# Kernel tuning notes

Hardware: AMD Instinct MI355X
Metric: run time of the kernel (lower is better)

Reference implementation:

```python
import jax, jax.numpy as jnp
import numpy as np


def setup_inputs() -> dict:
    key = jax.random.key(0)
    k1, k2 = jax.random.split(key)
    D, N, M = 256, 1024, 1024
    z_x = jax.random.normal(k1, (1, D, N), dtype=jnp.float32)
    z_y = jax.random.normal(k2, (1, D, M), dtype=jnp.float32)
    return {"z_x": z_x, "z_y": z_y}


def reference(z_x, z_y):
    # squeeze().t(): (1, d, N) -> (N, d)
    x = jnp.squeeze(z_x).T  # (N, d)
    y = jnp.squeeze(z_y).T  # (M, d)
    # L1 compare: s[i, j] = -sum_d |x[i, d] - y[j, d]|  -> (N, M)
    s = -jnp.sum(jnp.abs(x[:, None, :] - y[None, :, :]), axis=-1)
    a = jax.nn.softmax(s, axis=1)  # row-wise softmax
    b = jax.nn.softmax(s, axis=0)  # column-wise softmax
    a = a + b - a * b              # soft union of alignments
    return jnp.sum(a * s) / jnp.sum(a)
```

## Files before the change

### kernel.cpp

```cpp
#include <hip/hip_runtime.h>
#include <math.h>


#define DD 256
#define NN 1024
#define DS 4
#define CH (DD / DS)

__device__ __forceinline__ float waveMax(float v) {
  #pragma unroll
  for (int off = 32; off; off >>= 1) v = fmaxf(v, __shfl_xor(v, off, 64));
  return v;
}
__device__ __forceinline__ float waveSum(float v) {
  #pragma unroll
  for (int off = 32; off; off >>= 1) v += __shfl_xor(v, off, 64);
  return v;
}
__device__ __forceinline__ float blockMax(float v, float* red) {
  v = waveMax(v);
  __syncthreads();
  if ((threadIdx.x & 63) == 0) red[threadIdx.x >> 6] = v;
  __syncthreads();
  return fmaxf(fmaxf(red[0], red[1]), fmaxf(red[2], red[3]));
}
__device__ __forceinline__ float blockSum(float v, float* red) {
  v = waveSum(v);
  __syncthreads();
  if ((threadIdx.x & 63) == 0) red[threadIdx.x >> 6] = v;
  __syncthreads();
  return red[0] + red[1] + red[2] + red[3];
}


__global__ __launch_bounds__(256)
void scompute_kernel(const float* __restrict__ zx, const float* __restrict__ zy,
                     float* __restrict__ Sp, float* __restrict__ accum) {
  const int h  = blockIdx.z;
  const int i0 = blockIdx.y * 64;
  const int j0 = blockIdx.x * 128;
  const int t  = threadIdx.x;
  const int g  = t >> 5;
  const int c  = t & 31;
  if ((blockIdx.x | blockIdx.y | blockIdx.z) == 0 && t == 0) {
    accum[0] = 0.f; accum[1] = 0.f;
  }

  __shared__ float xs[CH * 64];
  {
    const float4* __restrict__ X4 = (const float4*)zx;
    float4* xs4 = (float4*)xs;
    #pragma unroll
    for (int k = t; k < CH * 16; k += 256)
      xs4[k] = X4[(h * CH + (k >> 4)) * (NN / 4) + (i0 >> 2) + (k & 15)];
  }
  __syncthreads();

  float acc[8][4];
  #pragma unroll
  for (int r = 0; r < 8; ++r)
    #pragma unroll
    for (int q = 0; q < 4; ++q) acc[r][q] = 0.f;

  const float4* __restrict__ yp =
      (const float4*)zy + (size_t)(h * CH) * (NN / 4) + (j0 >> 2) + c;
  #pragma unroll 4
  for (int d = 0; d < CH; ++d) {
    const float4 yv = yp[d * (NN / 4)];
    const float* xr = xs + d * 64 + g * 8;
    #pragma unroll
    for (int r = 0; r < 8; ++r) {
      const float xv = xr[r];
      acc[r][0] += fabsf(xv - yv.x);
      acc[r][1] += fabsf(xv - yv.y);
      acc[r][2] += fabsf(xv - yv.z);
      acc[r][3] += fabsf(xv - yv.w);
    }
  }

  float4* __restrict__ S4 = (float4*)Sp + (size_t)h * (NN * NN / 4);
  #pragma unroll
  for (int r = 0; r < 8; ++r)
    S4[(i0 + g * 8 + r) * (NN / 4) + (j0 >> 2) + c] =
        make_float4(acc[r][0], acc[r][1], acc[r][2], acc[r][3]);
}

__global__ __launch_bounds__(256)
void rowstats_kernel(float* __restrict__ Sp,
                     float* __restrict__ rmax, float* __restrict__ rsum) {
  __shared__ float red[4];
  const int t = threadIdx.x;
  const int row0 = blockIdx.x * 4;
  float4* S4 = (float4*)Sp;
  #pragma unroll
  for (int rr = 0; rr < 4; ++rr) {
    const int row = row0 + rr;
    float4 p = S4[row * (NN / 4) + t];
    #pragma unroll
    for (int hh = 1; hh < DS; ++hh) {
      const float4 q = S4[hh * (NN * NN / 4) + row * (NN / 4) + t];
      p.x += q.x; p.y += q.y; p.z += q.z; p.w += q.w;
    }
    S4[row * (NN / 4) + t] = p;
    float m = fmaxf(fmaxf(-p.x, -p.y), fmaxf(-p.z, -p.w));
    m = blockMax(m, red);
    float l = __expf(-p.x - m) + __expf(-p.y - m) +
              __expf(-p.z - m) + __expf(-p.w - m);
    l = blockSum(l, red);
    if (t == 0) { rmax[row] = m; rsum[row] = l; }
  }
}

__global__ __launch_bounds__(256)
void colstats_kernel(const float* __restrict__ Sp,
                     float* __restrict__ pm, float* __restrict__ ps) {
  const int t = threadIdx.x;
  const int r0 = blockIdx.x * 16;
  const float4* S4 = (const float4*)Sp;
  float4 m = make_float4(-1e30f, -1e30f, -1e30f, -1e30f);
  #pragma unroll 4
  for (int i = 0; i < 16; ++i) {
    const float4 p = S4[(r0 + i) * (NN / 4) + t];
    m.x = fmaxf(m.x, -p.x); m.y = fmaxf(m.y, -p.y);
    m.z = fmaxf(m.z, -p.z); m.w = fmaxf(m.w, -p.w);
  }
  float4 l = make_float4(0.f, 0.f, 0.f, 0.f);
  #pragma unroll 4
  for (int i = 0; i < 16; ++i) {
    const float4 p = S4[(r0 + i) * (NN / 4) + t];
    l.x += __expf(-p.x - m.x); l.y += __expf(-p.y - m.y);
    l.z += __expf(-p.z - m.z); l.w += __expf(-p.w - m.w);
  }
  ((float4*)pm)[blockIdx.x * (NN / 4) + t] = m;
  ((float4*)ps)[blockIdx.x * (NN / 4) + t] = l;
}

__global__ __launch_bounds__(256)
void colcombine_kernel(const float* __restrict__ pm, const float* __restrict__ ps,
                       float* __restrict__ cmax, float* __restrict__ csum) {
  const int j = blockIdx.x * 256 + threadIdx.x;
  float m = -1e30f;
  #pragma unroll 8
  for (int k = 0; k < 64; ++k) m = fmaxf(m, pm[k * NN + j]);
  float l = 0.f;
  #pragma unroll 8
  for (int k = 0; k < 64; ++k) l += __expf(pm[k * NN + j] - m) * ps[k * NN + j];
  cmax[j] = m; csum[j] = l;
}

__global__ __launch_bounds__(256)
void final_kernel(const float* __restrict__ Sp,
                  const float* __restrict__ rmax, const float* __restrict__ rsum,
                  const float* __restrict__ cmax, const float* __restrict__ csum,
                  float* __restrict__ accum) {
  __shared__ float redn[4], redd[4];
  const int t = threadIdx.x;
  const int row0 = blockIdx.x * 4;
  const float4* S4 = (const float4*)Sp;
  const float4 cm = ((const float4*)cmax)[t];
  const float4 cs = ((const float4*)csum)[t];
  float un = 0.f, ud = 0.f;
  #pragma unroll
  for (int rr = 0; rr < 4; ++rr) {
    const int row = row0 + rr;
    const float rm = rmax[row];
    const float ri = 1.f / rsum[row];
    const float4 p = S4[row * (NN / 4) + t];
    {
      const float s = -p.x;
      const float a = __expf(s - rm) * ri;
      const float b = __expf(s - cm.x) / cs.x;
      const float u = a + b - a * b;
      un += u * s; ud += u;
    }
    {
      const float s = -p.y;
      const float a = __expf(s - rm) * ri;
      const float b = __expf(s - cm.y) / cs.y;
      const float u = a + b - a * b;
      un += u * s; ud += u;
    }
    {
      const float s = -p.z;
      const float a = __expf(s - rm) * ri;
      const float b = __expf(s - cm.z) / cs.z;
      const float u = a + b - a * b;
      un += u * s; ud += u;
    }
    {
      const float s = -p.w;
      const float a = __expf(s - rm) * ri;
      const float b = __expf(s - cm.w) / cs.w;
      const float u = a + b - a * b;
      un += u * s; ud += u;
    }
  }
  un = waveSum(un); ud = waveSum(ud);
  if ((t & 63) == 0) { redn[t >> 6] = un; redd[t >> 6] = ud; }
  __syncthreads();
  if (t == 0) {
    atomicAdd(&accum[0], redn[0] + redn[1] + redn[2] + redn[3]);
    atomicAdd(&accum[1], redd[0] + redd[1] + redd[2] + redd[3]);
  }
}

__global__ void finalize_kernel(const float* __restrict__ accum, float* __restrict__ out) {
  out[0] = accum[0] / accum[1];
}


#define TJ  128
#define NCH (NN / TJ)
#define BLK 256

__global__ __launch_bounds__(BLK)
void stats2_kernel(const float* __restrict__ zx, const float* __restrict__ zy,
                   float* __restrict__ partM, float* __restrict__ partS) {
  const int side = blockIdx.z;
  const float* __restrict__ X = side ? zy : zx;
  const float* __restrict__ Y = side ? zx : zy;
  const int j0 = blockIdx.x * TJ;
  const int i0 = blockIdx.y * 8;
  const int t  = threadIdx.x;
  const int rg = t >> 5;
  const int c  = t & 31;

  __shared__ float xs[8 * DD];
  for (int k = t; k < 8 * DD; k += BLK)
    xs[k] = X[(k >> 3) * NN + i0 + (k & 7)];
  __syncthreads();

  const float4* __restrict__ Y4 = (const float4*)Y;
  const int yb = (j0 >> 2) + c;
  float4 acc = make_float4(0.f, 0.f, 0.f, 0.f);
  #pragma unroll 8
  for (int d = 0; d < DD; ++d) {
    const float4 yv = Y4[d * (NN / 4) + yb];
    const float xv = xs[d * 8 + rg];
    acc.x += fabsf(xv - yv.x);
    acc.y += fabsf(xv - yv.y);
    acc.z += fabsf(xv - yv.z);
    acc.w += fabsf(xv - yv.w);
  }

  float m = fmaxf(fmaxf(-acc.x, -acc.y), fmaxf(-acc.z, -acc.w));
  #pragma unroll
  for (int off = 16; off > 0; off >>= 1) m = fmaxf(m, __shfl_xor(m, off, 32));
  float p = __expf(-acc.x - m) + __expf(-acc.y - m) +
            __expf(-acc.z - m) + __expf(-acc.w - m);
  #pragma unroll
  for (int off = 16; off > 0; off >>= 1) p += __shfl_xor(p, off, 32);

  if (c == 0) {
    const int idx = side * (NCH * NN) + blockIdx.x * NN + (i0 + rg);
    partM[idx] = m;
    partS[idx] = p;
  }
}

__global__ __launch_bounds__(BLK)
void combine_kernel(const float* __restrict__ partM, const float* __restrict__ partS,
                    float* __restrict__ rmax, float* __restrict__ rsum,
                    float* __restrict__ cmax, float* __restrict__ csum,
                    float* __restrict__ accum) {
  const int gid = blockIdx.x * BLK + threadIdx.x;
  if (gid == 0) { accum[0] = 0.f; accum[1] = 0.f; }
  const int sd = gid >> 10;
  const int i  = gid & (NN - 1);
  float mk[NCH], sk[NCH];
  #pragma unroll
  for (int k = 0; k < NCH; ++k) {
    mk[k] = partM[sd * (NCH * NN) + k * NN + i];
    sk[k] = partS[sd * (NCH * NN) + k * NN + i];
  }
  float m = mk[0];
  #pragma unroll
  for (int k = 1; k < NCH; ++k) m = fmaxf(m, mk[k]);
  float s = 0.f;
  #pragma unroll
  for (int k = 0; k < NCH; ++k) s += __expf(mk[k] - m) * sk[k];
  if (sd == 0) { rmax[i] = m; rsum[i] = s; }
  else         { cmax[i] = m; csum[i] = s; }
}

__global__ __launch_bounds__(BLK)
void final2_kernel(const float* __restrict__ zx, const float* __restrict__ zy,
                   const float* __restrict__ rmax, const float* __restrict__ rsum,
                   const float* __restrict__ cmax, const float* __restrict__ csum,
                   float* __restrict__ accum) {
  const int j0 = blockIdx.x * TJ;
  const int i0 = blockIdx.y * 8;
  const int t  = threadIdx.x;
  const int rg = t >> 5;
  const int c  = t & 31;

  __shared__ float xs[8 * DD];
  __shared__ float redn[4], redd[4];
  for (int k = t; k < 8 * DD; k += BLK)
    xs[k] = zx[(k >> 3) * NN + i0 + (k & 7)];
  __syncthreads();

  const float4* __restrict__ Y4 = (const float4*)zy;
  const int yb = (j0 >> 2) + c;
  float4 acc = make_float4(0.f, 0.f, 0.f, 0.f);
  #pragma unroll 8
  for (int d = 0; d < DD; ++d) {
    const float4 yv = Y4[d * (NN / 4) + yb];
    const float xv = xs[d * 8 + rg];
    acc.x += fabsf(xv - yv.x);
    acc.y += fabsf(xv - yv.y);
    acc.z += fabsf(xv - yv.z);
    acc.w += fabsf(xv - yv.w);
  }

  const int i = i0 + rg;
  const float rm = rmax[i];
  const float ri = 1.f / rsum[i];
  const float4 cm = ((const float4*)cmax)[yb];
  const float4 cs = ((const float4*)csum)[yb];

  float un = 0.f, ud = 0.f;
  {
    const float s = -acc.x;
    const float a = __expf(s - rm) * ri;
    const float b = __expf(s - cm.x) / cs.x;
    const float u = a + b - a * b;
    un += u * s; ud += u;
  }
  {
    const float s = -acc.y;
    const float a = __expf(s - rm) * ri;
    const float b = __expf(s - cm.y) / cs.y;
    const float u = a + b - a * b;
    un += u * s; ud += u;
  }
  {
    const float s = -acc.z;
    const float a = __expf(s - rm) * ri;
    const float b = __expf(s - cm.z) / cs.z;
    const float u = a + b - a * b;
    un += u * s; ud += u;
  }
  {
    const float s = -acc.w;
    const float a = __expf(s - rm) * ri;
    const float b = __expf(s - cm.w) / cs.w;
    const float u = a + b - a * b;
    un += u * s; ud += u;
  }

  un = waveSum(un); ud = waveSum(ud);
  if ((t & 63) == 0) { redn[t >> 6] = un; redd[t >> 6] = ud; }
  __syncthreads();
  if (t == 0) {
    atomicAdd(&accum[0], redn[0] + redn[1] + redn[2] + redn[3]);
    atomicAdd(&accum[1], redd[0] + redd[1] + redd[2] + redd[3]);
  }
}


extern "C" void kernel_launch(void* const* d_in, const int* in_sizes, int n_in,
                              void* d_out, int out_size, void* d_ws, size_t ws_size,
                              hipStream_t stream) {
  const float* zx = (const float*)d_in[0];
  const float* zy = (const float*)d_in[1];
  float* ws  = (float*)d_ws;
  float* out = (float*)d_out;

  float* accum = ws;
  float* Sp    = ws + 16;
  float* pm    = Sp + DS * NN * NN;
  float* ps    = pm + 64 * NN;
  float* rmax  = ps + 64 * NN;
  float* rsum  = rmax + NN;
  float* cmax  = rsum + NN;
  float* csum  = cmax + NN;
  const size_t need = (size_t)((csum + NN) - ws) * sizeof(float);

  if (ws_size >= need) {
    dim3 g1(NN / 128, NN / 64, DS);
    scompute_kernel<<<g1, 256, 0, stream>>>(zx, zy, Sp, accum);
    rowstats_kernel<<<NN / 4, 256, 0, stream>>>(Sp, rmax, rsum);
    colstats_kernel<<<NN / 16, 256, 0, stream>>>(Sp, pm, ps);
    colcombine_kernel<<<NN / 256, 256, 0, stream>>>(pm, ps, cmax, csum);
    final_kernel<<<NN / 4, 256, 0, stream>>>(Sp, rmax, rsum, cmax, csum, accum);
    finalize_kernel<<<1, 1, 0, stream>>>(accum, out);
  } else {
    float* partM = ws + 16;
    float* partS = partM + 2 * NCH * NN;
    float* frmax = partS + 2 * NCH * NN;
    float* frsum = frmax + NN;
    float* fcmax = frsum + NN;
    float* fcsum = fcmax + NN;
    dim3 sgrid(NCH, NN / 8, 2);
    stats2_kernel<<<sgrid, BLK, 0, stream>>>(zx, zy, partM, partS);
    combine_kernel<<<(2 * NN) / BLK, BLK, 0, stream>>>(partM, partS,
                                                       frmax, frsum, fcmax, fcsum, accum);
    dim3 fgrid(NCH, NN / 8);
    final2_kernel<<<fgrid, BLK, 0, stream>>>(zx, zy, frmax, frsum, fcmax, fcsum, accum);
    finalize_kernel<<<1, 1, 0, stream>>>(accum, out);
  }
}
```

Baseline: 125.2 us.

## Fuse row/column softmax partial stats into distance kernel, drop split-D partials

The L1 distance kernel now computes the full D reduction per tile and a single S matrix, with Y tiles double-buffered in shared memory. It also emits per-tile row and column max/sum-exp partials, which removes the separate rowstats and colstats passes and the reads of four partial S copies. A single combine kernel merges the partials. The final kernel finishes the division through a last-block atomic counter, which drops the finalize launch. The grid shrinks to 256 blocks with launch_bounds(256,1), so occupancy and parallelism may be low relative to the earlier 512-block split-D launch.

Result: slower. 127.8 us (+2.1%).

```diff
diff --git a/kernel.cpp b/kernel.cpp
--- a/kernel.cpp
+++ b/kernel.cpp
@@ -4,8 +4,7 @@
 
 #define DD 256
 #define NN 1024
-#define DS 4
-#define CH (DD / DS)
+#define NQ 256
 
 __device__ __forceinline__ float waveMax(float v) {
   #pragma unroll
@@ -17,155 +16,168 @@
   for (int off = 32; off; off >>= 1) v += __shfl_xor(v, off, 64);
   return v;
 }
-__device__ __forceinline__ float blockMax(float v, float* red) {
-  v = waveMax(v);
-  __syncthreads();
-  if ((threadIdx.x & 63) == 0) red[threadIdx.x >> 6] = v;
-  __syncthreads();
-  return fmaxf(fmaxf(red[0], red[1]), fmaxf(red[2], red[3]));
-}
-__device__ __forceinline__ float blockSum(float v, float* red) {
-  v = waveSum(v);
-  __syncthreads();
-  if ((threadIdx.x & 63) == 0) red[threadIdx.x >> 6] = v;
-  __syncthreads();
-  return red[0] + red[1] + red[2] + red[3];
-}
-
+
+
+__global__ __launch_bounds__(256, 1)
+void scompute_kernel(const float* __restrict__ zx, const float* __restrict__ zy,
+                     float* __restrict__ S,
+                     float* __restrict__ pRM, float* __restrict__ pRL,
+                     float* __restrict__ pCM, float* __restrict__ pCL) {
+  const int bx = blockIdx.x;
+  const int by = blockIdx.y;
+  const int i0 = by * 16;
+  const int t  = threadIdx.x;
+  const int w  = t >> 6;
+  const int ln = t & 63;
+
+  __shared__ float xs[DD][16];
+  __shared__ float ys[2][8][256];
+  __shared__ float cmS[4][256];
+  __shared__ float clS[4][256];
+
+  const float4* __restrict__ X4 = (const float4*)zx;
+  const float4* __restrict__ Y4 = (const float4*)zy;
+
+  #pragma unroll
+  for (int i = 0; i < 4; ++i) {
+    const int k = t + i * 256;
+    const int d = k >> 2, rq = k & 3;
+    *(float4*)&xs[d][rq * 4] = X4[d * NQ + by * 4 + rq];
+  }
+
+  const int sd = t >> 6;
+  const int sq = t & 63;
+  {
+    const float4 q0 = Y4[(sd)     * NQ + bx * 64 + sq];
+    const float4 q1 = Y4[(4 + sd) * NQ + bx * 64 + sq];
+    *(float4*)&ys[0][sd][sq * 4]     = q0;
+    *(float4*)&ys[0][4 + sd][sq * 4] = q1;
+  }
+  __syncthreads();
+
+  float acc[4][4];
+  #pragma unroll
+  for (int r = 0; r < 4; ++r)
+    #pragma unroll
+    for (int c = 0; c < 4; ++c) acc[r][c] = 0.f;
+
+  #pragma unroll 1
+  for (int n = 0; n < DD / 8; ++n) {
+    const int buf = n & 1;
+    float4 p0, p1;
+    if (n < DD / 8 - 1) {
+      p0 = Y4[(8 * (n + 1) + sd)     * NQ + bx * 64 + sq];
+      p1 = Y4[(8 * (n + 1) + 4 + sd) * NQ + bx * 64 + sq];
+    }
+    #pragma unroll
+    for (int dd = 0; dd < 8; ++dd) {
+      const int d = n * 8 + dd;
+      const float4 xv = *(const float4*)&xs[d][w * 4];
+      const float4 yv = *(const float4*)&ys[buf][dd][ln * 4];
+      acc[0][0] += fabsf(xv.x - yv.x); acc[0][1] += fabsf(xv.x - yv.y);
+      acc[0][2] += fabsf(xv.x - yv.z); acc[0][3] += fabsf(xv.x - yv.w);
+      acc[1][0] += fabsf(xv.y - yv.x); acc[1][1] += fabsf(xv.y - yv.y);
+      acc[1][2] += fabsf(xv.y - yv.z); acc[1][3] += fabsf(xv.y - yv.w);
+      acc[2][0] += fabsf(xv.z - yv.x); acc[2][1] += fabsf(xv.z - yv.y);
+      acc[2][2] += fabsf(xv.z - yv.z); acc[2][3] += fabsf(xv.z - yv.w);
+      acc[3][0] += fabsf(xv.w - yv.x); acc[3][1] += fabsf(xv.w - yv.y);
+      acc[3][2] += fabsf(xv.w - yv.z); acc[3][3] += fabsf(xv.w - yv.w);
+    }
+    if (n < DD / 8 - 1) {
+      *(float4*)&ys[buf ^ 1][sd][sq * 4]     = p0;
+      *(float4*)&ys[buf ^ 1][4 + sd][sq * 4] = p1;
+    }
+    __syncthreads();
+  }
+
+  float4* __restrict__ S4 = (float4*)S;
+  #pragma unroll
+  for (int r = 0; r < 4; ++r)
+    S4[(i0 + w * 4 + r) * NQ + bx * 64 + ln] =
+        make_float4(acc[r][0], acc[r][1], acc[r][2], acc[r][3]);
+
+  #pragma unroll
+  for (int r = 0; r < 4; ++r) {
+    float m = fmaxf(fmaxf(-acc[r][0], -acc[r][1]), fmaxf(-acc[r][2], -acc[r][3]));
+    m = waveMax(m);
+    float l = __expf(-acc[r][0] - m) + __expf(-acc[r][1] - m) +
+              __expf(-acc[r][2] - m) + __expf(-acc[r][3] - m);
+    l = waveSum(l);
+    if (ln == 0) {
+      pRM[bx * NN + i0 + w * 4 + r] = m;
+      pRL[bx * NN + i0 + w * 4 + r] = l;
+    }
+  }
+
+  #pragma unroll
+  for (int c = 0; c < 4; ++c) {
+    float m = fmaxf(fmaxf(-acc[0][c], -acc[1][c]), fmaxf(-acc[2][c], -acc[3][c]));
+    float l = __expf(-acc[0][c] - m) + __expf(-acc[1][c] - m) +
+              __expf(-acc[2][c] - m) + __expf(-acc[3][c] - m);
+    cmS[w][ln * 4 + c] = m;
+    clS[w][ln * 4 + c] = l;
+  }
+  __syncthreads();
+  {
+    const int j = t;
+    const float m0 = cmS[0][j], m1 = cmS[1][j], m2 = cmS[2][j], m3 = cmS[3][j];
+    const float M = fmaxf(fmaxf(m0, m1), fmaxf(m2, m3));
+    const float L = clS[0][j] * __expf(m0 - M) + clS[1][j] * __expf(m1 - M) +
+                    clS[2][j] * __expf(m2 - M) + clS[3][j] * __expf(m3 - M);
+    pCM[by * NN + bx * 256 + j] = M;
+    pCL[by * NN + bx * 256 + j] = L;
+  }
+}
 
 __global__ __launch_bounds__(256)
-void scompute_kernel(const float* __restrict__ zx, const float* __restrict__ zy,
-                     float* __restrict__ Sp, float* __restrict__ accum) {
-  const int h  = blockIdx.z;
-  const int i0 = blockIdx.y * 64;
-  const int j0 = blockIdx.x * 128;
-  const int t  = threadIdx.x;
-  const int g  = t >> 5;
-  const int c  = t & 31;
-  if ((blockIdx.x | blockIdx.y | blockIdx.z) == 0 && t == 0) {
-    accum[0] = 0.f; accum[1] = 0.f;
-  }
-
-  __shared__ float xs[CH * 64];
-  {
-    const float4* __restrict__ X4 = (const float4*)zx;
-    float4* xs4 = (float4*)xs;
+void combine_kernel(const float* __restrict__ pRM, const float* __restrict__ pRL,
+                    const float* __restrict__ pCM, const float* __restrict__ pCL,
+                    float* __restrict__ rmax, float* __restrict__ rsum,
+                    float* __restrict__ cmax, float* __restrict__ csum,
+                    float* __restrict__ accum) {
+  const int b = blockIdx.x, t = threadIdx.x;
+  if (b == 0 && t == 0) {
+    accum[0] = 0.f; accum[1] = 0.f; ((unsigned int*)accum)[2] = 0u;
+  }
+  if (b < 4) {
+    const int r = b * 256 + t;
+    float mk[4], lk[4];
     #pragma unroll
-    for (int k = t; k < CH * 16; k += 256)
-      xs4[k] = X4[(h * CH + (k >> 4)) * (NN / 4) + (i0 >> 2) + (k & 15)];
-  }
-  __syncthreads();
-
-  float acc[8][4];
-  #pragma unroll
-  for (int r = 0; r < 8; ++r)
-    #pragma unroll
-    for (int q = 0; q < 4; ++q) acc[r][q] = 0.f;
-
-  const float4* __restrict__ yp =
-      (const float4*)zy + (size_t)(h * CH) * (NN / 4) + (j0 >> 2) + c;
-  #pragma unroll 4
-  for (int d = 0; d < CH; ++d) {
-    const float4 yv = yp[d * (NN / 4)];
-    const float* xr = xs + d * 64 + g * 8;
-    #pragma unroll
-    for (int r = 0; r < 8; ++r) {
-      const float xv = xr[r];
-      acc[r][0] += fabsf(xv - yv.x);
-      acc[r][1] += fabsf(xv - yv.y);
-      acc[r][2] += fabsf(xv - yv.z);
-      acc[r][3] += fabsf(xv - yv.w);
-    }
-  }
-
-  float4* __restrict__ S4 = (float4*)Sp + (size_t)h * (NN * NN / 4);
-  #pragma unroll
-  for (int r = 0; r < 8; ++r)
-    S4[(i0 + g * 8 + r) * (NN / 4) + (j0 >> 2) + c] =
-        make_float4(acc[r][0], acc[r][1], acc[r][2], acc[r][3]);
+    for (int k = 0; k < 4; ++k) { mk[k] = pRM[k * NN + r]; lk[k] = pRL[k * NN + r]; }
+    float m = fmaxf(fmaxf(mk[0], mk[1]), fmaxf(mk[2], mk[3]));
+    float l = lk[0] * __expf(mk[0] - m) + lk[1] * __expf(mk[1] - m) +
+              lk[2] * __expf(mk[2] - m) + lk[3] * __expf(mk[3] - m);
+    rmax[r] = m; rsum[r] = l;
+  } else {
+    const int j = (b - 4) * 256 + t;
+    float m = -1e30f;
+    #pragma unroll 8
+    for (int k = 0; k < 64; ++k) m = fmaxf(m, pCM[k * NN + j]);
+    float l = 0.f;
+    #pragma unroll 8
+    for (int k = 0; k < 64; ++k) l += __expf(pCM[k * NN + j] - m) * pCL[k * NN + j];
+    cmax[j] = m; csum[j] = l;
+  }
 }
 
 __global__ __launch_bounds__(256)
-void rowstats_kernel(float* __restrict__ Sp,
-                     float* __restrict__ rmax, float* __restrict__ rsum) {
-  __shared__ float red[4];
-  const int t = threadIdx.x;
-  const int row0 = blockIdx.x * 4;
-  float4* S4 = (float4*)Sp;
-  #pragma unroll
-  for (int rr = 0; rr < 4; ++rr) {
-    const int row = row0 + rr;
-    float4 p = S4[row * (NN / 4) + t];
-    #pragma unroll
-    for (int hh = 1; hh < DS; ++hh) {
-      const float4 q = S4[hh * (NN * NN / 4) + row * (NN / 4) + t];
-      p.x += q.x; p.y += q.y; p.z += q.z; p.w += q.w;
-    }
-    S4[row * (NN / 4) + t] = p;
-    float m = fmaxf(fmaxf(-p.x, -p.y), fmaxf(-p.z, -p.w));
-    m = blockMax(m, red);
-    float l = __expf(-p.x - m) + __expf(-p.y - m) +
-              __expf(-p.z - m) + __expf(-p.w - m);
-    l = blockSum(l, red);
-    if (t == 0) { rmax[row] = m; rsum[row] = l; }
-  }
-}
-
-__global__ __launch_bounds__(256)
-void colstats_kernel(const float* __restrict__ Sp,
-                     float* __restrict__ pm, float* __restrict__ ps) {
-  const int t = threadIdx.x;
-  const int r0 = blockIdx.x * 16;
-  const float4* S4 = (const float4*)Sp;
-  float4 m = make_float4(-1e30f, -1e30f, -1e30f, -1e30f);
-  #pragma unroll 4
-  for (int i = 0; i < 16; ++i) {
-    const float4 p = S4[(r0 + i) * (NN / 4) + t];
-    m.x = fmaxf(m.x, -p.x); m.y = fmaxf(m.y, -p.y);
-    m.z = fmaxf(m.z, -p.z); m.w = fmaxf(m.w, -p.w);
-  }
-  float4 l = make_float4(0.f, 0.f, 0.f, 0.f);
-  #pragma unroll 4
-  for (int i = 0; i < 16; ++i) {
-    const float4 p = S4[(r0 + i) * (NN / 4) + t];
-    l.x += __expf(-p.x - m.x); l.y += __expf(-p.y - m.y);
-    l.z += __expf(-p.z - m.z); l.w += __expf(-p.w - m.w);
-  }
-  ((float4*)pm)[blockIdx.x * (NN / 4) + t] = m;
-  ((float4*)ps)[blockIdx.x * (NN / 4) + t] = l;
-}
-
-__global__ __launch_bounds__(256)
-void colcombine_kernel(const float* __restrict__ pm, const float* __restrict__ ps,
-                       float* __restrict__ cmax, float* __restrict__ csum) {
-  const int j = blockIdx.x * 256 + threadIdx.x;
-  float m = -1e30f;
-  #pragma unroll 8
-  for (int k = 0; k < 64; ++k) m = fmaxf(m, pm[k * NN + j]);
-  float l = 0.f;
-  #pragma unroll 8
-  for (int k = 0; k < 64; ++k) l += __expf(pm[k * NN + j] - m) * ps[k * NN + j];
-  cmax[j] = m; csum[j] = l;
-}
-
-__global__ __launch_bounds__(256)
-void final_kernel(const float* __restrict__ Sp,
+void final_kernel(const float* __restrict__ S,
                   const float* __restrict__ rmax, const float* __restrict__ rsum,
                   const float* __restrict__ cmax, const float* __restrict__ csum,
-                  float* __restrict__ accum) {
+                  float* __restrict__ accum, float* __restrict__ out) {
   __shared__ float redn[4], redd[4];
   const int t = threadIdx.x;
-  const int row0 = blockIdx.x * 4;
-  const float4* S4 = (const float4*)Sp;
+  const int row0 = blockIdx.x * 2;
+  const float4* S4 = (const float4*)S;
   const float4 cm = ((const float4*)cmax)[t];
   const float4 cs = ((const float4*)csum)[t];
   float un = 0.f, ud = 0.f;
   #pragma unroll
-  for (int rr = 0; rr < 4; ++rr) {
-    const int row = row0 + rr;
+  for (int r = 0; r < 2; ++r) {
+    const int row = row0 + r;
     const float rm = rmax[row];
     const float ri = 1.f / rsum[row];
-    const float4 p = S4[row * (NN / 4) + t];
+    const float4 p = S4[row * NQ + t];
     {
       const float s = -p.x;
       const float a = __expf(s - rm) * ri;
@@ -201,11 +213,15 @@
   if (t == 0) {
     atomicAdd(&accum[0], redn[0] + redn[1] + redn[2] + redn[3]);
     atomicAdd(&accum[1], redd[0] + redd[1] + redd[2] + redd[3]);
-  }
-}
-
-__global__ void finalize_kernel(const float* __restrict__ accum, float* __restrict__ out) {
-  out[0] = accum[0] / accum[1];
+    __threadfence();
+    unsigned int* cnt = (unsigned int*)accum + 2;
+    const unsigned int old = atomicAdd(cnt, 1u);
+    if (old == gridDim.x - 1) {
+      const float n = atomicAdd(&accum[0], 0.f);
+      const float d = atomicAdd(&accum[1], 0.f);
+      out[0] = n / d;
+    }
+  }
 }
 
 
@@ -235,7 +251,7 @@
   float4 acc = make_float4(0.f, 0.f, 0.f, 0.f);
   #pragma unroll 8
   for (int d = 0; d < DD; ++d) {
-    const float4 yv = Y4[d * (NN / 4) + yb];
+    const float4 yv = Y4[d * NQ + yb];
     const float xv = xs[d * 8 + rg];
     acc.x += fabsf(xv - yv.x);
     acc.y += fabsf(xv - yv.y);
@@ -259,10 +275,10 @@
 }
 
 __global__ __launch_bounds__(BLK)
-void combine_kernel(const float* __restrict__ partM, const float* __restrict__ partS,
-                    float* __restrict__ rmax, float* __restrict__ rsum,
-                    float* __restrict__ cmax, float* __restrict__ csum,
-                    float* __restrict__ accum) {
+void combine_kernel_fb(const float* __restrict__ partM, const float* __restrict__ partS,
+                       float* __restrict__ rmax, float* __restrict__ rsum,
+                       float* __restrict__ cmax, float* __restrict__ csum,
+                       float* __restrict__ accum) {
   const int gid = blockIdx.x * BLK + threadIdx.x;
   if (gid == 0) { accum[0] = 0.f; accum[1] = 0.f; }
   const int sd = gid >> 10;
@@ -305,7 +321,7 @@
   float4 acc = make_float4(0.f, 0.f, 0.f, 0.f);
   #pragma unroll 8
   for (int d = 0; d < DD; ++d) {
-    const float4 yv = Y4[d * (NN / 4) + yb];
+    const float4 yv = Y4[d * NQ + yb];
     const float xv = xs[d * 8 + rg];
     acc.x += fabsf(xv - yv.x);
     acc.y += fabsf(xv - yv.y);
@@ -356,6 +372,10 @@
     atomicAdd(&accum[0], redn[0] + redn[1] + redn[2] + redn[3]);
     atomicAdd(&accum[1], redd[0] + redd[1] + redd[2] + redd[3]);
   }
+}
+
+__global__ void finalize_kernel(const float* __restrict__ accum, float* __restrict__ out) {
+  out[0] = accum[0] / accum[1];
 }
 
 
@@ -368,23 +388,23 @@
   float* out = (float*)d_out;
 
   float* accum = ws;
-  float* Sp    = ws + 16;
-  float* pm    = Sp + DS * NN * NN;
-  float* ps    = pm + 64 * NN;
-  float* rmax  = ps + 64 * NN;
+  float* S     = ws + 16;
+  float* pRM   = S + NN * NN;
+  float* pRL   = pRM + 4 * NN;
+  float* pCM   = pRL + 4 * NN;
+  float* pCL   = pCM + 64 * NN;
+  float* rmax  = pCL + 64 * NN;
   float* rsum  = rmax + NN;
   float* cmax  = rsum + NN;
   float* csum  = cmax + NN;
   const size_t need = (size_t)((csum + NN) - ws) * sizeof(float);
 
   if (ws_size >= need) {
-    dim3 g1(NN / 128, NN / 64, DS);
-    scompute_kernel<<<g1, 256, 0, stream>>>(zx, zy, Sp, accum);
-    rowstats_kernel<<<NN / 4, 256, 0, stream>>>(Sp, rmax, rsum);
-    colstats_kernel<<<NN / 16, 256, 0, stream>>>(Sp, pm, ps);
-    colcombine_kernel<<<NN / 256, 256, 0, stream>>>(pm, ps, cmax, csum);
-    final_kernel<<<NN / 4, 256, 0, stream>>>(Sp, rmax, rsum, cmax, csum, accum);
-    finalize_kernel<<<1, 1, 0, stream>>>(accum, out);
+    dim3 g1(4, 64);
+    scompute_kernel<<<g1, 256, 0, stream>>>(zx, zy, S, pRM, pRL, pCM, pCL);
+    combine_kernel<<<8, 256, 0, stream>>>(pRM, pRL, pCM, pCL,
+                                          rmax, rsum, cmax, csum, accum);
+    final_kernel<<<NN / 2, 256, 0, stream>>>(S, rmax, rsum, cmax, csum, accum, out);
   } else {
     float* partM = ws + 16;
     float* partS = partM + 2 * NCH * NN;
@@ -394,8 +414,8 @@
     float* fcsum = fcmax + NN;
     dim3 sgrid(NCH, NN / 8, 2);
     stats2_kernel<<<sgrid, BLK, 0, stream>>>(zx, zy, partM, partS);
-    combine_kernel<<<(2 * NN) / BLK, BLK, 0, stream>>>(partM, partS,
-                                                       frmax, frsum, fcmax, fcsum, accum);
+    combine_kernel_fb<<<(2 * NN) / BLK, BLK, 0, stream>>>(partM, partS,
+                                                          frmax, frsum, fcmax, fcsum, accum);
     dim3 fgrid(NCH, NN / 8);
     final2_kernel<<<fgrid, BLK, 0, stream>>>(zx, zy, frmax, frsum, fcmax, fcsum, accum);
     finalize_kernel<<<1, 1, 0, stream>>>(accum, out);
```
